# Kernel optimization log

Measured on AMD Instinct MI355X. Metric: run time of the kernel, lower is better.

Reference implementation:

```python
import jax, jax.numpy as jnp
import numpy as np

BS, VARNUM, EMB_DIM, SEED_DIM, N_HEADS = 32, 16384, 128, 128, 16


def setup_inputs() -> dict:
    key = jax.random.key(0)
    k1, k2, k3, k4 = jax.random.split(key, 4)
    query_seed = jax.random.normal(k1, (BS, SEED_DIM), dtype=jnp.float32)
    embeddings = jax.random.normal(k2, (BS, VARNUM, EMB_DIM), dtype=jnp.float32)
    # mask over varnum//2 base variables; 1 = keep, 0 = mask out
    attn_mask = jax.random.randint(k3, (BS, VARNUM // 2), 0, 2, dtype=jnp.int32)
    # xavier_normal_ init: std = sqrt(2 / (fan_in + fan_out))
    xavier_std = float(np.sqrt(2.0 / (EMB_DIM + SEED_DIM)))
    w_qs = jax.random.normal(k4, (N_HEADS, EMB_DIM, SEED_DIM), dtype=jnp.float32) * xavier_std
    return {"query_seed": query_seed, "embeddings": embeddings,
            "attn_mask": attn_mask, "w_qs": w_qs}


def _l2_normalize(x):
    # x / ||x||_2 along last dim (no eps, matching torch source)
    return x / jnp.linalg.norm(x, axis=-1, keepdims=True)


def reference(query_seed, embeddings, attn_mask, w_qs):
    bs, varnum, emb_dim = embeddings.shape
    n_heads = w_qs.shape[0]

    norm_embs = _l2_normalize(embeddings)                      # [bs, varnum, emb]
    # mm(w_qs.view(-1, seed), seed.T).T.view(bs, n_heads, emb) == einsum
    qs = jnp.tanh(jnp.einsum("hes,bs->bhe", w_qs, query_seed))  # [bs, heads, emb]
    norm_qs = _l2_normalize(qs)

    # orthogonality loss between head queries
    gram = jnp.einsum("bhe,bge->bhg", norm_qs, norm_qs)        # [bs, h, h]
    diff = gram - jnp.eye(n_heads, dtype=gram.dtype)
    loss = jnp.sum(diff * diff) / bs

    # cosine-similarity attention
    attn = jnp.einsum("bhe,bve->bhv", norm_qs, norm_embs)      # [bs, h, varnum]
    mask_full = jnp.concatenate([attn_mask, attn_mask], axis=1)[:, None, :]  # [bs,1,varnum]
    attn = jnp.where(mask_full == 0, -jnp.inf, attn)
    final_attn = jax.nn.softmax(attn, axis=-1)
    rc = jnp.einsum("bhv,bve->bhe", final_attn, embeddings)    # values = embeddings
    return rc, loss
```

## Files before the change

### kernel.cpp

```cpp
#include <hip/hip_runtime.h>
#include <hip/hip_bf16.h>
#include <cstdint>

#define BS     32
#define VARNUM 16384
#define EMB    128
#define SEEDD  128
#define NH     16
#define HALFV  8192

#define NCHUNK 32
#define VT     (VARNUM / NCHUNK)
#define TV     64
#define NTILE  (VT / TV)

#define EST 2080
#define PST 144

#define OFF_NORMQ 0
#define SZ_NORMQ  (BS*NH*EMB*4)
#define OFF_LOSSP (OFF_NORMQ + SZ_NORMQ)
#define SZ_LOSSP  256
#define OFF_LPART (OFF_LOSSP + SZ_LOSSP)
#define SZ_LPART  (BS*NCHUNK*NH*4)
#define OFF_PACC  (OFF_LPART + SZ_LPART)
#define SZ_PACC   ((size_t)BS*NCHUNK*NH*EMB*4)

typedef __attribute__((ext_vector_type(8))) short bf16x8;
typedef __attribute__((ext_vector_type(4))) float f32x4;

#define BAR() do { \
    asm volatile("s_waitcnt lgkmcnt(0)" ::: "memory"); \
    __builtin_amdgcn_s_barrier(); \
} while (0)

static __device__ __forceinline__ uint16_t f2bf(float f) {
    uint32_t u = __float_as_uint(f);
    return (uint16_t)((u + 0x7FFFu + ((u >> 16) & 1u)) >> 16);
}
static __device__ __forceinline__ uint32_t packbf(float a, float b) {
    __hip_bfloat162 h = __float22bfloat162_rn(make_float2(a, b));
    uint32_t u;
    __builtin_memcpy(&u, &h, 4);
    return u;
}
static __device__ __forceinline__ float dot4(float4 a, float4 b) {
    return a.x*b.x + a.y*b.y + a.z*b.z + a.w*b.w;
}

__global__ __launch_bounds__(128) void k1_q(const float* __restrict__ seed,
                                            const float* __restrict__ wqs,
                                            float* __restrict__ normq) {
    const int bh = blockIdx.x;
    const int b = bh >> 4, h = bh & 15;
    const int e = threadIdx.x;
    __shared__ __align__(16) float s_seed[SEEDD];
    s_seed[e] = seed[b*SEEDD + e];
    __syncthreads();
    const float4* w4 = (const float4*)(wqs + ((size_t)(h*EMB + e))*SEEDD);
    const float4* s4 = (const float4*)s_seed;
    float acc = 0.f;
    #pragma unroll
    for (int j = 0; j < SEEDD/4; ++j) acc += dot4(w4[j], s4[j]);
    float t = tanhf(acc);
    float sq = t*t;
    #pragma unroll
    for (int off = 32; off; off >>= 1) sq += __shfl_xor(sq, off);
    __shared__ float s_part[2];
    if ((threadIdx.x & 63) == 0) s_part[threadIdx.x >> 6] = sq;
    __syncthreads();
    float tot = s_part[0] + s_part[1];
    normq[((size_t)b*NH + h)*EMB + e] = t * rsqrtf(tot);
}

__global__ __launch_bounds__(256) void k2_loss(const float* __restrict__ normq,
                                               float* __restrict__ lossp) {
    const int b = blockIdx.x;
    const int h = threadIdx.x >> 4, g = threadIdx.x & 15;
    const float4* qh = (const float4*)(normq + ((size_t)b*NH + h)*EMB);
    const float4* qg = (const float4*)(normq + ((size_t)b*NH + g)*EMB);
    float d = 0.f;
    #pragma unroll
    for (int j = 0; j < EMB/4; ++j) d += dot4(qh[j], qg[j]);
    d -= (h == g) ? 1.f : 0.f;
    float sq = d*d;
    #pragma unroll
    for (int off = 32; off; off >>= 1) sq += __shfl_xor(sq, off);
    __shared__ float sp[4];
    if ((threadIdx.x & 63) == 0) sp[threadIdx.x >> 6] = sq;
    __syncthreads();
    if (threadIdx.x == 0) lossp[b] = sp[0] + sp[1] + sp[2] + sp[3];
}

__global__ __launch_bounds__(256, 4) void k_fused(const float* __restrict__ emb,
                                                  const int* __restrict__ mask,
                                                  const float* __restrict__ normq,
                                                  float* __restrict__ pacc,
                                                  float* __restrict__ lpart) {
    const int chunk = blockIdx.x, b = blockIdx.y;
    const int tid = threadIdx.x;
    const int w   = tid >> 6;
    const int l   = tid & 63;
    const int lhi = l >> 4;
    const int llo = l & 15;
    const int rr  = w*16 + llo;

    __shared__ __align__(16) unsigned char Elds[2][8*EST];
    __shared__ __align__(16) unsigned char Plds[2][16*PST];
    __shared__ __align__(16) float nsq[TV];
    __shared__ float lred[4][NH];

    bf16x8 qf[4];
    {
        const float* qrow = normq + ((size_t)b*NH + llo)*EMB;
        #pragma unroll
        for (int f = 0; f < 4; ++f) {
            const float4* qs = (const float4*)(qrow + f*32 + lhi*8);
            float4 a = qs[0], c = qs[1];
            bf16x8 t;
            t[0]=(short)f2bf(a.x); t[1]=(short)f2bf(a.y); t[2]=(short)f2bf(a.z); t[3]=(short)f2bf(a.w);
            t[4]=(short)f2bf(c.x); t[5]=(short)f2bf(c.y); t[6]=(short)f2bf(c.z); t[7]=(short)f2bf(c.w);
            qf[f] = t;
        }
    }

    f32x4 acc0 = {0.f,0.f,0.f,0.f};
    f32x4 acc1 = {0.f,0.f,0.f,0.f};
    float Lh = 0.f;

    const float* embB  = emb + (size_t)b*VARNUM*EMB;
    const int*   maskB = mask + b*HALFV;

    int    mk;
    float4 pfa[4], pfb[4];
    {
        const int vg = chunk*VT + rr;
        mk = maskB[vg & (HALFV-1)];
        const float* rowp = embB + (size_t)(mk ? vg : (chunk*VT + w*16))*EMB;
        #pragma unroll
        for (int f = 0; f < 4; ++f) {
            const float4* src = (const float4*)(rowp + f*32 + lhi*8);
            pfa[f] = src[0]; pfb[f] = src[1];
        }
    }

    for (int t = 0; t < NTILE; ++t) {
        unsigned char* Ebuf = Elds[t & 1];
        unsigned char* Pbuf = Plds[t & 1];

        int mkn = 0;
        if (t + 1 < NTILE)
            mkn = maskB[(chunk*VT + (t+1)*TV + rr) & (HALFV-1)];

        bf16x8 ef[4];
        float sq = 0.f;
        #pragma unroll
        for (int f = 0; f < 4; ++f) {
            float4 x0 = pfa[f], x1 = pfb[f];
            sq += dot4(x0,x0) + dot4(x1,x1);
            uint4 dd = make_uint4(packbf(x0.x,x0.y), packbf(x0.z,x0.w),
                                  packbf(x1.x,x1.y), packbf(x1.z,x1.w));
            *(uint4*)(Ebuf + (2*f + (lhi>>1))*EST + rr*32 + (lhi&1)*16) = dd;
            __builtin_memcpy(&ef[f], &dd, 16);
        }
        sq += __shfl_xor(sq, 16);
        sq += __shfl_xor(sq, 32);
        if (l < 16) nsq[w*16 + llo] = mk ? sq : 0.f;

        if (t + 1 < NTILE) {
            const int vg = chunk*VT + (t+1)*TV + rr;
            const float* rowp = embB + (size_t)(mkn ? vg : (chunk*VT + (t+1)*TV + w*16))*EMB;
            #pragma unroll
            for (int f = 0; f < 4; ++f) {
                const float4* src = (const float4*)(rowp + f*32 + lhi*8);
                pfa[f] = src[0]; pfb[f] = src[1];
            }
            mk = mkn;
        }

        f32x4 s = {0.f,0.f,0.f,0.f};
        #pragma unroll
        for (int f = 0; f < 4; ++f)
            s = __builtin_amdgcn_mfma_f32_16x16x32_bf16(ef[f], qf[f], s, 0, 0, 0);

        f32x4 nn = *(const f32x4*)(&nsq[w*16 + lhi*4]);
        float p[4];
        #pragma unroll
        for (int r = 0; r < 4; ++r)
            p[r] = (nn[r] > 0.f) ? __expf(s[r]*rsqrtf(nn[r]) - 1.f) : 0.f;
        uint32_t u0 = packbf(p[0], p[1]), u1 = packbf(p[2], p[3]);
        Lh += __uint_as_float(u0 << 16) + __uint_as_float(u0 & 0xFFFF0000u)
            + __uint_as_float(u1 << 16) + __uint_as_float(u1 & 0xFFFF0000u);
        {
            unsigned char* pdst = Pbuf + llo*PST + (w*16 + lhi*4)*2;
            *(uint32_t*)(pdst)     = u0;
            *(uint32_t*)(pdst + 4) = u1;
        }

        BAR();

        #pragma unroll
        for (int kf = 0; kf < 2; ++kf) {
            bf16x8 pa = *(const bf16x8*)(Pbuf + llo*PST + kf*64 + lhi*16);
            #pragma unroll
            for (int et = 0; et < 2; ++et) {
                const unsigned char* base = Ebuf + (2*w + et)*EST + llo*2;
                bf16x8 bb;
                #pragma unroll
                for (int i = 0; i < 8; ++i)
                    bb[i] = *(const short*)(base + (size_t)(kf*32 + lhi*8 + i)*32);
                if (et == 0) acc0 = __builtin_amdgcn_mfma_f32_16x16x32_bf16(pa, bb, acc0, 0, 0, 0);
                else         acc1 = __builtin_amdgcn_mfma_f32_16x16x32_bf16(pa, bb, acc1, 0, 0, 0);
            }
        }
    }

    float* pout = pacc + (((size_t)b*NCHUNK + chunk)*NH)*EMB;
    #pragma unroll
    for (int r = 0; r < 4; ++r) {
        pout[(lhi*4 + r)*EMB + w*32 + llo]      = acc0[r];
        pout[(lhi*4 + r)*EMB + w*32 + 16 + llo] = acc1[r];
    }
    Lh += __shfl_xor(Lh, 16);
    Lh += __shfl_xor(Lh, 32);
    if (l < 16) lred[w][l] = Lh;
    BAR();
    if (tid < 16)
        lpart[((size_t)b*NCHUNK + chunk)*NH + tid] =
            lred[0][tid] + lred[1][tid] + lred[2][tid] + lred[3][tid];
}

__global__ __launch_bounds__(128) void k6_out(const float* __restrict__ pacc,
                                              const float* __restrict__ lpart,
                                              const float* __restrict__ lossp,
                                              float* __restrict__ out) {
    const int bh = blockIdx.x;
    const int b = bh >> 4, h = bh & 15;
    const int e = threadIdx.x;
    float L = 0.f;
    #pragma unroll
    for (int c = 0; c < NCHUNK; ++c) L += lpart[((size_t)b*NCHUNK + c)*NH + h];
    float acc = 0.f;
    for (int k = 0; k < NCHUNK; ++k)
        acc += pacc[(((size_t)b*NCHUNK + k)*NH + h)*EMB + e];
    out[((size_t)b*NH + h)*EMB + e] = acc / L;
    if (bh == 0 && e < 64) {
        float v = (e < BS) ? lossp[e] : 0.f;
        #pragma unroll
        for (int off = 32; off; off >>= 1) v += __shfl_xor(v, off);
        if (e == 0) out[BS*NH*EMB] = v / (float)BS;
    }
}

extern "C" void kernel_launch(void* const* d_in, const int* in_sizes, int n_in,
                              void* d_out, int out_size, void* d_ws, size_t ws_size,
                              hipStream_t stream) {
    const float* seed = (const float*)d_in[0];
    const float* emb  = (const float*)d_in[1];
    const int*   mask = (const int*)d_in[2];
    const float* wqs  = (const float*)d_in[3];
    float* out = (float*)d_out;

    char* ws = (char*)d_ws;
    float* normq = (float*)(ws + OFF_NORMQ);
    float* lossp = (float*)(ws + OFF_LOSSP);
    float* lpart = (float*)(ws + OFF_LPART);
    float* pacc  = (float*)(ws + OFF_PACC);

    k1_q<<<BS*NH, 128, 0, stream>>>(seed, wqs, normq);
    k2_loss<<<BS, 256, 0, stream>>>(normq, lossp);
    k_fused<<<dim3(NCHUNK, BS), 256, 0, stream>>>(emb, mask, normq, pacc, lpart);
    k6_out<<<BS*NH, 128, 0, stream>>>(pacc, lpart, lossp, out);
}
```

Before: 50.66 us.

## Compact unmasked row indices and stream only kept embedding rows

Adds a pre-pass kernel that builds, per batch, a compacted list of kept variable indices (each base index paired with its mirrored half) using a prefix scan over the mask. The fused attention kernel then splits the kept rows evenly across chunks and loops over only those rows, instead of walking every row and substituting a dummy row for masked ones. This removes the MFMA and exp work spent on masked rows and balances work across chunks, at the cost of an extra launch, an index buffer, and an indirect (gathered) load per row.

```diff
diff --git a/kernel.cpp b/kernel.cpp
--- a/kernel.cpp
+++ b/kernel.cpp
@@ -10,9 +10,7 @@
 #define HALFV  8192
 
 #define NCHUNK 32
-#define VT     (VARNUM / NCHUNK)
 #define TV     64
-#define NTILE  (VT / TV)
 
 #define EST 2080
 #define PST 144
@@ -23,7 +21,11 @@
 #define SZ_LOSSP  256
 #define OFF_LPART (OFF_LOSSP + SZ_LOSSP)
 #define SZ_LPART  (BS*NCHUNK*NH*4)
-#define OFF_PACC  (OFF_LPART + SZ_LPART)
+#define OFF_CNT   (OFF_LPART + SZ_LPART)
+#define SZ_CNT    256
+#define OFF_AIDX  (OFF_CNT + SZ_CNT)
+#define SZ_AIDX   ((size_t)BS*VARNUM*4)
+#define OFF_PACC  (OFF_AIDX + SZ_AIDX)
 #define SZ_PACC   ((size_t)BS*NCHUNK*NH*EMB*4)
 
 typedef __attribute__((ext_vector_type(8))) short bf16x8;
@@ -46,6 +48,47 @@
 }
 static __device__ __forceinline__ float dot4(float4 a, float4 b) {
     return a.x*b.x + a.y*b.y + a.z*b.z + a.w*b.w;
+}
+
+__global__ __launch_bounds__(256) void k0_compact(const int* __restrict__ mask,
+                                                  int* __restrict__ aidx,
+                                                  int* __restrict__ cntv) {
+    const int b = blockIdx.x;
+    const int tid = threadIdx.x;
+    const int base = tid * 32;
+    const int* m = mask + (size_t)b*HALFV;
+    int lc = 0;
+    uint32_t bits = 0;
+    #pragma unroll 8
+    for (int j = 0; j < 32; ++j) {
+        int mm = m[base + j] & 1;
+        bits |= (uint32_t)mm << j;
+        lc += mm;
+    }
+    const int lane = tid & 63, wv = tid >> 6;
+    int x = lc;
+    #pragma unroll
+    for (int off = 1; off < 64; off <<= 1) {
+        int y = __shfl_up(x, off);
+        if (lane >= off) x += y;
+    }
+    __shared__ int wsum[4];
+    if (lane == 63) wsum[wv] = x;
+    __syncthreads();
+    int wbase = 0;
+    #pragma unroll
+    for (int k = 0; k < 4; ++k) if (k < wv) wbase += wsum[k];
+    int pos = wbase + x - lc;
+    int* aB = aidx + (size_t)b*VARNUM;
+    for (int j = 0; j < 32; ++j) {
+        if ((bits >> j) & 1u) {
+            const int v = base + j;
+            aB[2*pos]     = v;
+            aB[2*pos + 1] = v + HALFV;
+            ++pos;
+        }
+    }
+    if (tid == 255) cntv[b] = 2 * (wbase + x);
 }
 
 __global__ __launch_bounds__(128) void k1_q(const float* __restrict__ seed,
@@ -93,7 +136,8 @@
 }
 
 __global__ __launch_bounds__(256, 4) void k_fused(const float* __restrict__ emb,
-                                                  const int* __restrict__ mask,
+                                                  const int* __restrict__ aidx,
+                                                  const int* __restrict__ cntv,
                                                   const float* __restrict__ normq,
                                                   float* __restrict__ pacc,
                                                   float* __restrict__ lpart) {
@@ -110,6 +154,13 @@
     __shared__ __align__(16) float nsq[TV];
     __shared__ float lred[4][NH];
 
+    const int cnt   = cntv[b];
+    const int sBeg  = (cnt * chunk) >> 5;
+    const int sEnd  = (cnt * (chunk + 1)) >> 5;
+    const int nrow  = sEnd - sBeg;
+    const int ntile = (nrow + TV - 1) >> 6;
+    const int* aB   = aidx + (size_t)b*VARNUM;
+
     bf16x8 qf[4];
     {
         const float* qrow = normq + ((size_t)b*NH + llo)*EMB;
@@ -128,15 +179,14 @@
     f32x4 acc1 = {0.f,0.f,0.f,0.f};
     float Lh = 0.f;
 
-    const float* embB  = emb + (size_t)b*VARNUM*EMB;
-    const int*   maskB = mask + b*HALFV;
-
-    int    mk;
+    const float* embB = emb + (size_t)b*VARNUM*EMB;
+
+    int    vld = 0;
     float4 pfa[4], pfb[4];
-    {
-        const int vg = chunk*VT + rr;
-        mk = maskB[vg & (HALFV-1)];
-        const float* rowp = embB + (size_t)(mk ? vg : (chunk*VT + w*16))*EMB;
+    if (ntile > 0) {
+        vld = rr < nrow;
+        const int vg = aB[sBeg + (vld ? rr : 0)];
+        const float* rowp = embB + (size_t)vg*EMB;
         #pragma unroll
         for (int f = 0; f < 4; ++f) {
             const float4* src = (const float4*)(rowp + f*32 + lhi*8);
@@ -144,13 +194,16 @@
         }
     }
 
-    for (int t = 0; t < NTILE; ++t) {
+    for (int t = 0; t < ntile; ++t) {
         unsigned char* Ebuf = Elds[t & 1];
         unsigned char* Pbuf = Plds[t & 1];
 
-        int mkn = 0;
-        if (t + 1 < NTILE)
-            mkn = maskB[(chunk*VT + (t+1)*TV + rr) & (HALFV-1)];
+        int vldn = 0, vgn = 0;
+        if (t + 1 < ntile) {
+            const int ii = (t + 1)*TV + rr;
+            vldn = ii < nrow;
+            vgn  = aB[sBeg + (vldn ? ii : 0)];
+        }
 
         bf16x8 ef[4];
         float sq = 0.f;
@@ -165,17 +218,16 @@
         }
         sq += __shfl_xor(sq, 16);
         sq += __shfl_xor(sq, 32);
-        if (l < 16) nsq[w*16 + llo] = mk ? sq : 0.f;
-
-        if (t + 1 < NTILE) {
-            const int vg = chunk*VT + (t+1)*TV + rr;
-            const float* rowp = embB + (size_t)(mkn ? vg : (chunk*VT + (t+1)*TV + w*16))*EMB;
+        if (l < 16) nsq[w*16 + llo] = vld ? sq : 0.f;
+
+        if (t + 1 < ntile) {
+            const float* rowp = embB + (size_t)vgn*EMB;
             #pragma unroll
             for (int f = 0; f < 4; ++f) {
                 const float4* src = (const float4*)(rowp + f*32 + lhi*8);
                 pfa[f] = src[0]; pfb[f] = src[1];
             }
-            mk = mkn;
+            vld = vldn;
         }
 
         f32x4 s = {0.f,0.f,0.f,0.f};
@@ -265,10 +317,13 @@
     float* normq = (float*)(ws + OFF_NORMQ);
     float* lossp = (float*)(ws + OFF_LOSSP);
     float* lpart = (float*)(ws + OFF_LPART);
+    int*   cntv  = (int*)(ws + OFF_CNT);
+    int*   aidx  = (int*)(ws + OFF_AIDX);
     float* pacc  = (float*)(ws + OFF_PACC);
 
     k1_q<<<BS*NH, 128, 0, stream>>>(seed, wqs, normq);
     k2_loss<<<BS, 256, 0, stream>>>(normq, lossp);
-    k_fused<<<dim3(NCHUNK, BS), 256, 0, stream>>>(emb, mask, normq, pacc, lpart);
+    k0_compact<<<BS, 256, 0, stream>>>(mask, aidx, cntv);
+    k_fused<<<dim3(NCHUNK, BS), 256, 0, stream>>>(emb, aidx, cntv, normq, pacc, lpart);
     k6_out<<<BS*NH, 128, 0, stream>>>(pacc, lpart, lossp, out);
 }
```

Result: slower. 53.41 us (+5.4%).

## Make each wave own its vocab sub-tile and drop per-tile block barriers

Applied to the files above, without the earlier changes.

Each wave now handles the P·E product for its own 16 rows across all 128 embedding columns, using 16x16x16 bf16 MFMAs over eight accumulators. Because a wave only reads the LDS sub-tile it wrote itself, the shared P buffer and the block-wide barrier on every tile are gone. The four per-wave partial outputs are reduced through LDS once at the end. The cost is more accumulator registers, twice as many smaller MFMAs, and a final cross-wave reduction in LDS.

```diff
diff --git a/kernel.cpp b/kernel.cpp
--- a/kernel.cpp
+++ b/kernel.cpp
@@ -14,8 +14,9 @@
 #define TV     64
 #define NTILE  (VT / TV)
 
-#define EST 2080
-#define PST 144
+#define RST 40
+#define SST 640
+#define WSUB (8*SST)
 
 #define OFF_NORMQ 0
 #define SZ_NORMQ  (BS*NH*EMB*4)
@@ -27,12 +28,8 @@
 #define SZ_PACC   ((size_t)BS*NCHUNK*NH*EMB*4)
 
 typedef __attribute__((ext_vector_type(8))) short bf16x8;
+typedef __attribute__((ext_vector_type(4))) short s16x4;
 typedef __attribute__((ext_vector_type(4))) float f32x4;
-
-#define BAR() do { \
-    asm volatile("s_waitcnt lgkmcnt(0)" ::: "memory"); \
-    __builtin_amdgcn_s_barrier(); \
-} while (0)
 
 static __device__ __forceinline__ uint16_t f2bf(float f) {
     uint32_t u = __float_as_uint(f);
@@ -46,6 +43,17 @@
 }
 static __device__ __forceinline__ float dot4(float4 a, float4 b) {
     return a.x*b.x + a.y*b.y + a.z*b.z + a.w*b.w;
+}
+
+static __device__ __forceinline__ f32x4 mfma16(s16x4 a, s16x4 b, f32x4 c) {
+#if __has_builtin(__builtin_amdgcn_mfma_f32_16x16x16bf16_1k)
+    return __builtin_amdgcn_mfma_f32_16x16x16bf16_1k(a, b, c, 0, 0, 0);
+#elif __has_builtin(__builtin_amdgcn_mfma_f32_16x16x16_bf16)
+    return __builtin_amdgcn_mfma_f32_16x16x16_bf16(a, b, c, 0, 0, 0);
+#else
+    asm("v_mfma_f32_16x16x16_bf16 %0, %1, %2, %0" : "+v"(c) : "v"(a), "v"(b));
+    return c;
+#endif
 }
 
 __global__ __launch_bounds__(128) void k1_q(const float* __restrict__ seed,
@@ -105,10 +113,11 @@
     const int llo = l & 15;
     const int rr  = w*16 + llo;
 
-    __shared__ __align__(16) unsigned char Elds[2][8*EST];
-    __shared__ __align__(16) unsigned char Plds[2][16*PST];
-    __shared__ __align__(16) float nsq[TV];
+    __shared__ __align__(16) unsigned char SMEM[4*NH*EMB*4];
     __shared__ float lred[4][NH];
+
+    unsigned char* subt = SMEM + w*WSUB;
+    float*         nsqw = (float*)(SMEM + 4*WSUB) + w*16;
 
     bf16x8 qf[4];
     {
@@ -124,8 +133,9 @@
         }
     }
 
-    f32x4 acc0 = {0.f,0.f,0.f,0.f};
-    f32x4 acc1 = {0.f,0.f,0.f,0.f};
+    f32x4 acc[8];
+    #pragma unroll
+    for (int et = 0; et < 8; ++et) acc[et] = (f32x4){0.f,0.f,0.f,0.f};
     float Lh = 0.f;
 
     const float* embB  = emb + (size_t)b*VARNUM*EMB;
@@ -145,9 +155,6 @@
     }
 
     for (int t = 0; t < NTILE; ++t) {
-        unsigned char* Ebuf = Elds[t & 1];
-        unsigned char* Pbuf = Plds[t & 1];
-
         int mkn = 0;
         if (t + 1 < NTILE)
             mkn = maskB[(chunk*VT + (t+1)*TV + rr) & (HALFV-1)];
@@ -158,14 +165,17 @@
         for (int f = 0; f < 4; ++f) {
             float4 x0 = pfa[f], x1 = pfb[f];
             sq += dot4(x0,x0) + dot4(x1,x1);
-            uint4 dd = make_uint4(packbf(x0.x,x0.y), packbf(x0.z,x0.w),
-                                  packbf(x1.x,x1.y), packbf(x1.z,x1.w));
-            *(uint4*)(Ebuf + (2*f + (lhi>>1))*EST + rr*32 + (lhi&1)*16) = dd;
-            __builtin_memcpy(&ef[f], &dd, 16);
+            uint2 lo = make_uint2(packbf(x0.x,x0.y), packbf(x0.z,x0.w));
+            uint2 hi = make_uint2(packbf(x1.x,x1.y), packbf(x1.z,x1.w));
+            unsigned char* wp = subt + (2*f + (lhi>>1))*SST + llo*RST + (lhi&1)*16;
+            *(uint2*)(wp)     = lo;
+            *(uint2*)(wp + 8) = hi;
+            __builtin_memcpy(&ef[f], &lo, 8);
+            __builtin_memcpy(((char*)&ef[f]) + 8, &hi, 8);
         }
         sq += __shfl_xor(sq, 16);
         sq += __shfl_xor(sq, 32);
-        if (l < 16) nsq[w*16 + llo] = mk ? sq : 0.f;
+        if (l < 16) nsqw[llo] = mk ? sq : 0.f;
 
         if (t + 1 < NTILE) {
             const int vg = chunk*VT + (t+1)*TV + rr;
@@ -183,48 +193,54 @@
         for (int f = 0; f < 4; ++f)
             s = __builtin_amdgcn_mfma_f32_16x16x32_bf16(ef[f], qf[f], s, 0, 0, 0);
 
-        f32x4 nn = *(const f32x4*)(&nsq[w*16 + lhi*4]);
+        f32x4 nn = *(const f32x4*)(&nsqw[lhi*4]);
         float p[4];
         #pragma unroll
         for (int r = 0; r < 4; ++r)
             p[r] = (nn[r] > 0.f) ? __expf(s[r]*rsqrtf(nn[r]) - 1.f) : 0.f;
-        uint32_t u0 = packbf(p[0], p[1]), u1 = packbf(p[2], p[3]);
-        Lh += __uint_as_float(u0 << 16) + __uint_as_float(u0 & 0xFFFF0000u)
-            + __uint_as_float(u1 << 16) + __uint_as_float(u1 & 0xFFFF0000u);
-        {
-            unsigned char* pdst = Pbuf + llo*PST + (w*16 + lhi*4)*2;
-            *(uint32_t*)(pdst)     = u0;
-            *(uint32_t*)(pdst + 4) = u1;
-        }
-
-        BAR();
-
-        #pragma unroll
-        for (int kf = 0; kf < 2; ++kf) {
-            bf16x8 pa = *(const bf16x8*)(Pbuf + llo*PST + kf*64 + lhi*16);
+        uint32_t u01[2] = { packbf(p[0], p[1]), packbf(p[2], p[3]) };
+        Lh += __uint_as_float(u01[0] << 16) + __uint_as_float(u01[0] & 0xFFFF0000u)
+            + __uint_as_float(u01[1] << 16) + __uint_as_float(u01[1] & 0xFFFF0000u);
+        s16x4 pa;
+        __builtin_memcpy(&pa, u01, 8);
+
+        const unsigned char* rb = subt + lhi*(4*RST) + llo*2;
+        #pragma unroll
+        for (int et = 0; et < 8; ++et) {
+            s16x4 bb;
             #pragma unroll
-            for (int et = 0; et < 2; ++et) {
-                const unsigned char* base = Ebuf + (2*w + et)*EST + llo*2;
-                bf16x8 bb;
-                #pragma unroll
-                for (int i = 0; i < 8; ++i)
-                    bb[i] = *(const short*)(base + (size_t)(kf*32 + lhi*8 + i)*32);
-                if (et == 0) acc0 = __builtin_amdgcn_mfma_f32_16x16x32_bf16(pa, bb, acc0, 0, 0, 0);
-                else         acc1 = __builtin_amdgcn_mfma_f32_16x16x32_bf16(pa, bb, acc1, 0, 0, 0);
-            }
-        }
-    }
-
-    float* pout = pacc + (((size_t)b*NCHUNK + chunk)*NH)*EMB;
-    #pragma unroll
-    for (int r = 0; r < 4; ++r) {
-        pout[(lhi*4 + r)*EMB + w*32 + llo]      = acc0[r];
-        pout[(lhi*4 + r)*EMB + w*32 + 16 + llo] = acc1[r];
-    }
+            for (int i = 0; i < 4; ++i)
+                bb[i] = *(const short*)(rb + et*SST + i*RST);
+            acc[et] = mfma16(pa, bb, acc[et]);
+        }
+    }
+
     Lh += __shfl_xor(Lh, 16);
     Lh += __shfl_xor(Lh, 32);
-    if (l < 16) lred[w][l] = Lh;
-    BAR();
+    if (l < 16) lred[w][llo] = Lh;
+    __syncthreads();
+
+    float* Ow = (float*)SMEM + w*(NH*EMB);
+    #pragma unroll
+    for (int et = 0; et < 8; ++et)
+        #pragma unroll
+        for (int r = 0; r < 4; ++r)
+            Ow[(lhi*4 + r)*EMB + et*16 + llo] = acc[et][r];
+    __syncthreads();
+
+    {
+        const float* S0 = (float*)SMEM;
+        f32x4 v0 = *(const f32x4*)(S0 + 0*(NH*EMB) + tid*8);
+        f32x4 v1 = *(const f32x4*)(S0 + 0*(NH*EMB) + tid*8 + 4);
+        #pragma unroll
+        for (int ww = 1; ww < 4; ++ww) {
+            v0 += *(const f32x4*)(S0 + ww*(NH*EMB) + tid*8);
+            v1 += *(const f32x4*)(S0 + ww*(NH*EMB) + tid*8 + 4);
+        }
+        float* pout = pacc + (((size_t)b*NCHUNK + chunk)*NH)*EMB;
+        *(f32x4*)(pout + tid*8)     = v0;
+        *(f32x4*)(pout + tid*8 + 4) = v1;
+    }
     if (tid < 16)
         lpart[((size_t)b*NCHUNK + chunk)*NH + tid] =
             lred[0][tid] + lred[1][tid] + lred[2][tid] + lred[3][tid];
```

New measurement: 57.31 us. +13.1%, slower.
